# Kernel optimization log

Measured on AMD Instinct MI355X. Metric: run time of the kernel, lower is better.

## Reference

```python
import jax, jax.numpy as jnp
import numpy as np

B, T, D, H = 64, 196, 768, 3072
WBIT_MAX = 127.0          # int8 symmetric weight range
BIAS_MAX = 2.0 ** 31 - 1  # bias_bit = 32


def round_ste(v):
    # straight-through rounding (QAT semantics)
    return v + jax.lax.stop_gradient(jnp.round(v) - v)


def quant_linear(x, w, b, a_s, relu_clip):
    # symmetric per-tensor int8 weight quantization
    w_s = jnp.max(jnp.abs(w)) / WBIT_MAX
    w_int = jnp.clip(round_ste(w / w_s), -WBIT_MAX, WBIT_MAX)
    # bias quantized at the accumulator scale a_s * w_s (int32 range)
    b_int = jnp.clip(round_ste(b / (w_s * a_s)), -BIAS_MAX, BIAS_MAX)
    out = jnp.einsum('btd,hd->bth', x, w_int) + b_int  # integer-domain accumulation
    if relu_clip:
        out = jax.nn.relu(out)
    return out, w_s, a_s * w_s


def setup_inputs() -> dict:
    key = jax.random.key(0)
    ks = jax.random.split(key, 6)
    x = jnp.round(jax.random.normal(ks[0], (B, T, D), dtype=jnp.float32) * 20.0)  # int8-like activations
    w1 = jax.random.normal(ks[1], (H, D), dtype=jnp.float32) * 0.02
    b1 = jax.random.normal(ks[2], (H,), dtype=jnp.float32) * 0.02
    w2 = jax.random.normal(ks[3], (D, H), dtype=jnp.float32) * 0.02
    b2 = jax.random.normal(ks[4], (D,), dtype=jnp.float32) * 0.02
    a_s = jax.random.uniform(ks[5], (1,), dtype=jnp.float32, minval=0.01, maxval=0.05)
    return {"x": x, "w1": w1, "b1": b1, "w2": w2, "b2": b2, "a_s": a_s}


def reference(x, w1, b1, w2, b2, a_s):
    s = a_s[0]
    # fc1: quantized linear, no activation clip
    h, w_s1, s = quant_linear(x, w1, b1, s, relu_clip=False)
    # fc2: quantized linear with ReLU clip
    out, w_s2, s = quant_linear(h, w2, b2, s, relu_clip=True)
    return (out, s)
```

## Files before the change

### kernel.cpp

```cpp
#include <hip/hip_runtime.h>
#include <hip/hip_bf16.h>
#include <type_traits>

typedef __attribute__((ext_vector_type(4))) float f32x4;
typedef __attribute__((ext_vector_type(4))) int   i32x4;

static __device__ __forceinline__ void stage16(const void* g, void* l) {
  __builtin_amdgcn_global_load_lds((const __attribute__((address_space(1))) void*)g,
                                   (__attribute__((address_space(3))) void*)l,
                                   16, 0, 0);
}

__global__ void prep_kernel(const float4* __restrict__ x, uchar4* __restrict__ xq, int n4x,
                            const float4* __restrict__ w1, const float4* __restrict__ w2,
                            int n4w, unsigned* __restrict__ mx) {
  if (blockIdx.y == 0) {
    const int stride = gridDim.x * blockDim.x;
    for (int i = blockIdx.x * blockDim.x + threadIdx.x; i < n4x; i += stride) {
      float4 v = x[i];
      uchar4 o;
      o.x = (unsigned char)(char)fminf(fmaxf(v.x, -127.f), 127.f);
      o.y = (unsigned char)(char)fminf(fmaxf(v.y, -127.f), 127.f);
      o.z = (unsigned char)(char)fminf(fmaxf(v.z, -127.f), 127.f);
      o.w = (unsigned char)(char)fminf(fmaxf(v.w, -127.f), 127.f);
      xq[i] = o;
    }
  } else {
    if (blockIdx.x >= 96) return;
    __shared__ unsigned red[4];
    const float4* w = (blockIdx.y == 1) ? w1 : w2;
    unsigned m = 0;
    const int stride = 96 * 256;
    for (int i = blockIdx.x * blockDim.x + threadIdx.x; i < n4w; i += stride) {
      float4 v = w[i];
      unsigned a;
      a = __float_as_uint(fabsf(v.x)); m = m > a ? m : a;
      a = __float_as_uint(fabsf(v.y)); m = m > a ? m : a;
      a = __float_as_uint(fabsf(v.z)); m = m > a ? m : a;
      a = __float_as_uint(fabsf(v.w)); m = m > a ? m : a;
    }
#pragma unroll
    for (int off = 32; off > 0; off >>= 1) {
      unsigned t = (unsigned)__shfl_down((int)m, off, 64);
      m = m > t ? m : t;
    }
    if ((threadIdx.x & 63) == 0) red[threadIdx.x >> 6] = m;
    __syncthreads();
    if (threadIdx.x == 0) {
      unsigned t0 = red[0] > red[1] ? red[0] : red[1];
      unsigned t1 = red[2] > red[3] ? red[2] : red[3];
      atomicMax(mx + blockIdx.y - 1, t0 > t1 ? t0 : t1);
    }
  }
}

__global__ void quantwb_kernel(const float* __restrict__ w1, const float* __restrict__ w2,
                               unsigned char* __restrict__ w1q, unsigned* __restrict__ w2qw,
                               const float* __restrict__ b1, const float* __restrict__ b2,
                               float* __restrict__ b1i, float* __restrict__ b2i,
                               const unsigned* __restrict__ mx, const float* __restrict__ a_s,
                               float* __restrict__ s_out, int n4, int H, int D) {
  const float ws1 = __uint_as_float(mx[0]) / 127.0f;
  const float ws2 = __uint_as_float(mx[1]) / 127.0f;
  const int stride = gridDim.x * blockDim.x;
  if (blockIdx.y == 0) {
    const float4* w = (const float4*)w1;
    uchar4* wq = (uchar4*)w1q;
    for (int i = blockIdx.x * blockDim.x + threadIdx.x; i < n4; i += stride) {
      float4 v = w[i];
      uchar4 o;
      o.x = (unsigned char)(char)fminf(fmaxf(rintf(v.x / ws1), -127.f), 127.f);
      o.y = (unsigned char)(char)fminf(fmaxf(rintf(v.y / ws1), -127.f), 127.f);
      o.z = (unsigned char)(char)fminf(fmaxf(rintf(v.z / ws1), -127.f), 127.f);
      o.w = (unsigned char)(char)fminf(fmaxf(rintf(v.w / ws1), -127.f), 127.f);
      wq[i] = o;
    }
  } else if (blockIdx.y == 1) {
    const int ndw = n4;
    const int dpr = H >> 2;
    for (int g = blockIdx.x * blockDim.x + threadIdx.x; g < ndw; g += stride) {
      const int n = g / dpr;
      const int d = g - n * dpr;
      const int grp = d >> 4, dl = d & 15;
      const float* src = w2 + (size_t)n * H + grp * 64 + dl;
      unsigned r = 0;
#pragma unroll
      for (int i = 0; i < 4; ++i) {
        float v = src[i * 16];
        int q = (int)fminf(fmaxf(rintf(v / ws2), -127.f), 127.f);
        r |= ((unsigned)q & 0xFFu) << (i * 8);
      }
      w2qw[g] = r;
    }
  } else {
    if (blockIdx.x != 0) return;
    const float s0 = a_s[0];
    const float s1 = s0 * ws1;
    const float d1 = ws1 * s0;
    const float d2 = ws2 * s1;
    if (threadIdx.x == 0) s_out[0] = s1 * ws2;
    for (int i = threadIdx.x; i < H; i += blockDim.x) {
      float q = rintf(b1[i] / d1);
      b1i[i] = fminf(fmaxf(q, -2147483647.f), 2147483647.f);
    }
    for (int i = threadIdx.x; i < D; i += blockDim.x) {
      float q = rintf(b2[i] / d2);
      b2i[i] = fminf(fmaxf(q, -2147483647.f), 2147483647.f);
    }
  }
}


__global__ __launch_bounds__(256) void gemm_fc1(
    const char* __restrict__ A, const char* __restrict__ Bt,
    const float* __restrict__ b1f, unsigned char* __restrict__ hq,
    float* __restrict__ stab, int M, int N, int Kb)
{
  __shared__ char lds[2 * 32768];
  const int tid = threadIdx.x;
  const int lane = tid & 63;
  const int wave = tid >> 6;
  const int wr = wave >> 1;
  const int wc = wave & 1;

  const int nbx = M / 128;
  const int nby = N / 128;
  const int bandSize = 16 * nby;
  const int b = blockIdx.x / bandSize;
  const int local = blockIdx.x - b * bandSize;
  const int r0 = b * 16;
  const int rn = min(16, nbx - r0);
  const int c = local / rn;
  const int r = r0 + (local - c * rn);
  const int row0 = r * 128;
  const int col0 = c * 128;

  const int srw = tid >> 3;
  const int chunk = (tid & 7) ^ (srw & 7);
  const char* Ag = A + (size_t)(row0 + srw) * Kb + chunk * 16;
  const char* Bg = Bt + (size_t)(col0 + srw) * Kb + chunk * 16;
  const int stA = wave * 1024;
  const int stB = 16384 + wave * 1024;

  auto stage = [&](int slot, int h) {
    const int hb = h << 7;
    char* da = lds + slot * 32768 + stA;
    char* db = lds + slot * 32768 + stB;
#pragma unroll
    for (int i = 0; i < 4; ++i)
      stage16(Ag + hb + (size_t)(i * 32) * Kb, da + i * 4096);
#pragma unroll
    for (int i = 0; i < 4; ++i)
      stage16(Bg + hb + (size_t)(i * 32) * Kb, db + i * 4096);
  };

  i32x4 acc[4][4];
#pragma unroll
  for (int i = 0; i < 4; ++i)
#pragma unroll
    for (int j = 0; j < 4; ++j) acc[i][j] = (i32x4)(0);

  const int nS = Kb >> 7;
  stage(0, 0);
  stage(1, 1);
  asm volatile("s_waitcnt vmcnt(8)" ::: "memory");
  __builtin_amdgcn_s_barrier();

  const int fr = lane & 15;
  const int fg = lane >> 4;
  const int xw = (fg ^ (fr & 7)) << 4;
  const int aoff = (wr * 64 + fr) * 128 + xw;
  const int boff = 16384 + (wc * 64 + fr) * 128 + xw;

  for (int t = 0; t < nS; ++t) {
    const int so = (t & 1) * 32768;
    i32x4 af[2][4], bf[2][4];
#pragma unroll
    for (int h = 0; h < 2; ++h) {
      const int hx = h << 6;
#pragma unroll
      for (int mi = 0; mi < 4; ++mi)
        af[h][mi] = *(const i32x4*)(lds + so + ((aoff ^ hx) + mi * 2048));
#pragma unroll
      for (int ni = 0; ni < 4; ++ni)
        bf[h][ni] = *(const i32x4*)(lds + so + ((boff ^ hx) + ni * 2048));
    }
    asm volatile("s_waitcnt lgkmcnt(0)" ::: "memory");
    __builtin_amdgcn_sched_barrier(0);
    __builtin_amdgcn_s_barrier();
    if (t + 2 < nS) stage(t & 1, t + 2);
    __builtin_amdgcn_s_setprio(1);
#pragma unroll
    for (int h = 0; h < 2; ++h)
#pragma unroll
      for (int mi = 0; mi < 4; ++mi)
#pragma unroll
        for (int ni = 0; ni < 4; ++ni)
          acc[mi][ni] = __builtin_amdgcn_mfma_i32_16x16x64_i8(
              af[h][mi], bf[h][ni], acc[mi][ni], 0, 0, 0);
    __builtin_amdgcn_s_setprio(0);
    if (t + 2 < nS) asm volatile("s_waitcnt vmcnt(8)" ::: "memory");
    else            asm volatile("s_waitcnt vmcnt(0)" ::: "memory");
    __builtin_amdgcn_s_barrier();
  }

  __syncthreads();
  float* rowtab = (float*)lds;
  const int orow_l = wr * 64 + fg * 4;
  const int ocol_l = wc * 64 + fr;
  float bv[4];
#pragma unroll
  for (int nf = 0; nf < 4; ++nf) bv[nf] = b1f[col0 + ocol_l + nf * 16];

#pragma unroll
  for (int mf = 0; mf < 4; ++mf) {
    float rmax[4] = {0.f, 0.f, 0.f, 0.f};
#pragma unroll
    for (int nf = 0; nf < 4; ++nf)
#pragma unroll
      for (int rg = 0; rg < 4; ++rg) {
        float v = (float)acc[mf][nf][rg] + bv[nf];
        rmax[rg] = fmaxf(rmax[rg], fabsf(v));
      }
#pragma unroll
    for (int rg = 0; rg < 4; ++rg) {
#pragma unroll
      for (int m = 1; m <= 8; m <<= 1)
        rmax[rg] = fmaxf(rmax[rg], __shfl_xor(rmax[rg], m, 64));
      if (fr == 0) rowtab[(orow_l + mf * 16 + rg) * 2 + wc] = rmax[rg];
    }
  }
  __syncthreads();
#pragma unroll
  for (int mf = 0; mf < 4; ++mf) {
#pragma unroll
    for (int rg = 0; rg < 4; ++rg) {
      const int lr = orow_l + mf * 16 + rg;
      float rm = fmaxf(rowtab[lr * 2], rowtab[lr * 2 + 1]);
      float inv = rm > 0.f ? 127.f / rm : 0.f;
      if (wc == 0 && fr == 0) stab[(size_t)(row0 + lr) * 24 + c] = rm * (1.f / 127.f);
      unsigned pk = 0;
#pragma unroll
      for (int nf = 0; nf < 4; ++nf) {
        float v = (float)acc[mf][nf][rg] + bv[nf];
        int q = (int)rintf(v * inv);
        pk |= ((unsigned)q & 0xFFu) << (nf * 8);
      }
      *(unsigned*)(hq + (size_t)(row0 + lr) * N + col0 + wc * 64 + fr * 4) = pk;
    }
  }
}

__global__ void requant_kernel(const uint4* __restrict__ hq, uint4* __restrict__ hq2,
                               const float* __restrict__ stab, float* __restrict__ srow,
                               int Mrows) {
  const int row = blockIdx.x * 4 + (threadIdx.x >> 6);
  if (row >= Mrows) return;
  const int lane = threadIdx.x & 63;
  const float* st = stab + (size_t)row * 24;
  float sr = 0.f;
#pragma unroll
  for (int i = 0; i < 24; ++i) sr = fmaxf(sr, st[i]);
  if (lane == 0) srow[row] = sr;
  const float rinv = sr > 0.f ? 1.f / sr : 0.f;
  const uint4* in = hq + (size_t)row * 192;
  uint4* outp = hq2 + (size_t)row * 192;
#pragma unroll
  for (int it = 0; it < 3; ++it) {
    const int j = lane + it * 64;
    const float ratio = st[j >> 3] * rinv;
    uint4 iv = in[j], ov;
    unsigned* ip = (unsigned*)&iv;
    unsigned* op = (unsigned*)&ov;
#pragma unroll
    for (int w = 0; w < 4; ++w) {
      unsigned rr = 0;
#pragma unroll
      for (int k = 0; k < 4; ++k) {
        int q = (int)(signed char)((ip[w] >> (k * 8)) & 0xFF);
        int nq = (int)rintf((float)q * ratio);
        rr |= ((unsigned)nq & 0xFF) << (k * 8);
      }
      op[w] = rr;
    }
    outp[j] = ov;
  }
}

__global__ __launch_bounds__(256) void gemm_fc2(
    const char* __restrict__ A, const char* __restrict__ Bt,
    const float* __restrict__ bias, const float* __restrict__ srow,
    float* __restrict__ Cout, int M, int N, int Kb)
{
  __shared__ char lds[2 * 32768];
  const int tid = threadIdx.x;
  const int lane = tid & 63;
  const int wave = tid >> 6;
  const int wr = wave >> 1;
  const int wc = wave & 1;

  const int nbx = M / 128;
  const int nby = N / 128;
  const int nwg = nbx * nby;
  const int q8 = nwg >> 3, r8 = nwg & 7;
  const int xcd = blockIdx.x & 7, bidx = blockIdx.x >> 3;
  const int wg = (xcd < r8 ? xcd * (q8 + 1) : r8 * (q8 + 1) + (xcd - r8) * q8) + bidx;
  const int r = wg / nby;
  const int c = wg % nby;
  const int row0 = r * 128;
  const int col0 = c * 128;

  const int srw = tid >> 3;
  const int chunk = (tid & 7) ^ (srw & 7);
  const char* Ag = A + (size_t)(row0 + srw) * Kb + chunk * 16;
  const char* Bg = Bt + (size_t)(col0 + srw) * Kb + chunk * 16;
  const int stA = wave * 1024;
  const int stB = 16384 + wave * 1024;

  auto stage = [&](int slot, int h) {
    const int hb = h << 7;
    char* da = lds + slot * 32768 + stA;
    char* db = lds + slot * 32768 + stB;
#pragma unroll
    for (int i = 0; i < 4; ++i)
      stage16(Ag + hb + (size_t)(i * 32) * Kb, da + i * 4096);
#pragma unroll
    for (int i = 0; i < 4; ++i)
      stage16(Bg + hb + (size_t)(i * 32) * Kb, db + i * 4096);
  };

  i32x4 acc[4][4];
#pragma unroll
  for (int i = 0; i < 4; ++i)
#pragma unroll
    for (int j = 0; j < 4; ++j) acc[i][j] = (i32x4)(0);

  const int nS = Kb >> 7;
  stage(0, 0);
  stage(1, 1);
  asm volatile("s_waitcnt vmcnt(8)" ::: "memory");
  __builtin_amdgcn_s_barrier();

  const int fr = lane & 15;
  const int fg = lane >> 4;
  const int xw = (fg ^ (fr & 7)) << 4;
  const int aoff = (wr * 64 + fr) * 128 + xw;
  const int boff = 16384 + (wc * 64 + fr) * 128 + xw;

  for (int t = 0; t < nS; ++t) {
    const int so = (t & 1) * 32768;
    i32x4 af[2][4], bf[2][4];
#pragma unroll
    for (int h = 0; h < 2; ++h) {
      const int hx = h << 6;
#pragma unroll
      for (int mi = 0; mi < 4; ++mi)
        af[h][mi] = *(const i32x4*)(lds + so + ((aoff ^ hx) + mi * 2048));
#pragma unroll
      for (int ni = 0; ni < 4; ++ni)
        bf[h][ni] = *(const i32x4*)(lds + so + ((boff ^ hx) + ni * 2048));
    }
    asm volatile("s_waitcnt lgkmcnt(0)" ::: "memory");
    __builtin_amdgcn_sched_barrier(0);
    __builtin_amdgcn_s_barrier();
    if (t + 2 < nS) stage(t & 1, t + 2);
    __builtin_amdgcn_s_setprio(1);
#pragma unroll
    for (int h = 0; h < 2; ++h)
#pragma unroll
      for (int mi = 0; mi < 4; ++mi)
#pragma unroll
        for (int ni = 0; ni < 4; ++ni)
          acc[mi][ni] = __builtin_amdgcn_mfma_i32_16x16x64_i8(
              af[h][mi], bf[h][ni], acc[mi][ni], 0, 0, 0);
    __builtin_amdgcn_s_setprio(0);
    if (t + 2 < nS) asm volatile("s_waitcnt vmcnt(8)" ::: "memory");
    else            asm volatile("s_waitcnt vmcnt(0)" ::: "memory");
    __builtin_amdgcn_s_barrier();
  }

  const int orow = row0 + wr * 64 + fg * 4;
  const int ocol = col0 + wc * 64 + fr;
#pragma unroll
  for (int mi = 0; mi < 4; ++mi) {
    float sr[4];
#pragma unroll
    for (int rg = 0; rg < 4; ++rg) sr[rg] = srow[orow + mi * 16 + rg];
#pragma unroll
    for (int ni = 0; ni < 4; ++ni) {
      const int col = ocol + ni * 16;
      const float bv = bias[col];
#pragma unroll
      for (int rg = 0; rg < 4; ++rg) {
        float v = sr[rg] * (float)acc[mi][ni][rg] + bv;
        Cout[(size_t)(orow + mi * 16 + rg) * N + col] = fmaxf(v, 0.f);
      }
    }
  }
}


extern "C" void kernel_launch(void* const* d_in, const int* in_sizes, int n_in,
                              void* d_out, int out_size, void* d_ws, size_t ws_size,
                              hipStream_t stream) {
  const float* x  = (const float*)d_in[0];
  const float* w1 = (const float*)d_in[1];
  const float* b1 = (const float*)d_in[2];
  const float* w2 = (const float*)d_in[3];
  const float* b2 = (const float*)d_in[4];
  const float* as = (const float*)d_in[5];

  const int Mrows = 64 * 196;
  const int D = 768, H = 3072;

  char* ws = (char*)d_ws;
  size_t off = 0;
  auto align256 = [](size_t v) { return (v + 255) & ~(size_t)255; };
  unsigned* mx = (unsigned*)(ws + off); off += 256;
  char* xq8    = (char*)(ws + off);     off += align256((size_t)Mrows * D);
  char* w1q8   = (char*)(ws + off);     off += align256((size_t)H * D);
  char* w2q8   = (char*)(ws + off);     off += align256((size_t)D * H);
  float* b1i = (float*)(ws + off); off += align256((size_t)H * 4);
  float* b2i = (float*)(ws + off); off += align256((size_t)D * 4);
  float* stab = (float*)(ws + off); off += align256((size_t)Mrows * 24 * 4);
  float* srow = (float*)(ws + off); off += align256((size_t)Mrows * 4);
  unsigned char* hq  = (unsigned char*)(ws + off); off += align256((size_t)Mrows * H);
  unsigned char* hq2 = (unsigned char*)(ws + off); off += align256((size_t)Mrows * H);
  if (off > ws_size) return;

  float* out = (float*)d_out;
  float* s_out = out + (out_size - 1);

  hipMemsetAsync(mx, 0, 8, stream);

  const int nw4 = H * D / 4;
  prep_kernel<<<dim3(1024, 3), dim3(256), 0, stream>>>(
      (const float4*)x, (uchar4*)xq8, Mrows * D / 4,
      (const float4*)w1, (const float4*)w2, nw4, mx);
  quantwb_kernel<<<dim3(1024, 3), dim3(256), 0, stream>>>(
      w1, w2, (unsigned char*)w1q8, (unsigned*)w2q8,
      b1, b2, b1i, b2i, mx, as, s_out, nw4, H, D);

  gemm_fc1<<<dim3((Mrows / 128) * (H / 128)), dim3(256), 0, stream>>>(
      xq8, w1q8, b1i, hq, stab, Mrows, H, D);
  requant_kernel<<<dim3(Mrows / 4), dim3(256), 0, stream>>>(
      (const uint4*)hq, (uint4*)hq2, stab, srow, Mrows);
  gemm_fc2<<<dim3((Mrows / 128) * (D / 128)), dim3(256), 0, stream>>>(
      (const char*)hq2, w2q8, b2i, srow, out, Mrows, D, H);
}
```

Before: 147.2 us.

## Single-buffer fc1 GEMM and move activation quantization into quantwb kernel

The fc1 GEMM drops its double-buffered LDS pipeline, where the next tile was prefetched while the current one was computed. It now loads one 32KB K-tile per iteration, synchronizes, runs the MFMAs, then synchronizes again, and keeps a separate 1KB region for the row-max table. The smaller LDS footprint could allow more blocks per CU, but global loads no longer overlap with compute, and there are two full barriers per K step. Separately, the x-to-int8 conversion moves from the max-reduction kernel into the quantwb kernel as a new grid row, so the reduction kernel launches only 96x2 blocks.

```diff
diff --git a/kernel.cpp b/kernel.cpp
--- a/kernel.cpp
+++ b/kernel.cpp
@@ -11,51 +11,37 @@
                                    16, 0, 0);
 }
 
-__global__ void prep_kernel(const float4* __restrict__ x, uchar4* __restrict__ xq, int n4x,
-                            const float4* __restrict__ w1, const float4* __restrict__ w2,
+__global__ void prep_kernel(const float4* __restrict__ w1, const float4* __restrict__ w2,
                             int n4w, unsigned* __restrict__ mx) {
-  if (blockIdx.y == 0) {
-    const int stride = gridDim.x * blockDim.x;
-    for (int i = blockIdx.x * blockDim.x + threadIdx.x; i < n4x; i += stride) {
-      float4 v = x[i];
-      uchar4 o;
-      o.x = (unsigned char)(char)fminf(fmaxf(v.x, -127.f), 127.f);
-      o.y = (unsigned char)(char)fminf(fmaxf(v.y, -127.f), 127.f);
-      o.z = (unsigned char)(char)fminf(fmaxf(v.z, -127.f), 127.f);
-      o.w = (unsigned char)(char)fminf(fmaxf(v.w, -127.f), 127.f);
-      xq[i] = o;
-    }
-  } else {
-    if (blockIdx.x >= 96) return;
-    __shared__ unsigned red[4];
-    const float4* w = (blockIdx.y == 1) ? w1 : w2;
-    unsigned m = 0;
-    const int stride = 96 * 256;
-    for (int i = blockIdx.x * blockDim.x + threadIdx.x; i < n4w; i += stride) {
-      float4 v = w[i];
-      unsigned a;
-      a = __float_as_uint(fabsf(v.x)); m = m > a ? m : a;
-      a = __float_as_uint(fabsf(v.y)); m = m > a ? m : a;
-      a = __float_as_uint(fabsf(v.z)); m = m > a ? m : a;
-      a = __float_as_uint(fabsf(v.w)); m = m > a ? m : a;
-    }
-#pragma unroll
-    for (int off = 32; off > 0; off >>= 1) {
-      unsigned t = (unsigned)__shfl_down((int)m, off, 64);
-      m = m > t ? m : t;
-    }
-    if ((threadIdx.x & 63) == 0) red[threadIdx.x >> 6] = m;
-    __syncthreads();
-    if (threadIdx.x == 0) {
-      unsigned t0 = red[0] > red[1] ? red[0] : red[1];
-      unsigned t1 = red[2] > red[3] ? red[2] : red[3];
-      atomicMax(mx + blockIdx.y - 1, t0 > t1 ? t0 : t1);
-    }
+  __shared__ unsigned red[4];
+  const float4* w = blockIdx.y ? w2 : w1;
+  unsigned m = 0;
+  const int stride = gridDim.x * blockDim.x;
+  for (int i = blockIdx.x * blockDim.x + threadIdx.x; i < n4w; i += stride) {
+    float4 v = w[i];
+    unsigned a;
+    a = __float_as_uint(fabsf(v.x)); m = m > a ? m : a;
+    a = __float_as_uint(fabsf(v.y)); m = m > a ? m : a;
+    a = __float_as_uint(fabsf(v.z)); m = m > a ? m : a;
+    a = __float_as_uint(fabsf(v.w)); m = m > a ? m : a;
+  }
+#pragma unroll
+  for (int off = 32; off > 0; off >>= 1) {
+    unsigned t = (unsigned)__shfl_down((int)m, off, 64);
+    m = m > t ? m : t;
+  }
+  if ((threadIdx.x & 63) == 0) red[threadIdx.x >> 6] = m;
+  __syncthreads();
+  if (threadIdx.x == 0) {
+    unsigned t0 = red[0] > red[1] ? red[0] : red[1];
+    unsigned t1 = red[2] > red[3] ? red[2] : red[3];
+    atomicMax(mx + blockIdx.y, t0 > t1 ? t0 : t1);
   }
 }
 
 __global__ void quantwb_kernel(const float* __restrict__ w1, const float* __restrict__ w2,
                                unsigned char* __restrict__ w1q, unsigned* __restrict__ w2qw,
+                               const float4* __restrict__ x, uchar4* __restrict__ xq, int n4x,
                                const float* __restrict__ b1, const float* __restrict__ b2,
                                float* __restrict__ b1i, float* __restrict__ b2i,
                                const unsigned* __restrict__ mx, const float* __restrict__ a_s,
@@ -92,6 +78,16 @@
       }
       w2qw[g] = r;
     }
+  } else if (blockIdx.y == 2) {
+    for (int i = blockIdx.x * blockDim.x + threadIdx.x; i < n4x; i += stride) {
+      float4 v = x[i];
+      uchar4 o;
+      o.x = (unsigned char)(char)fminf(fmaxf(v.x, -127.f), 127.f);
+      o.y = (unsigned char)(char)fminf(fmaxf(v.y, -127.f), 127.f);
+      o.z = (unsigned char)(char)fminf(fmaxf(v.z, -127.f), 127.f);
+      o.w = (unsigned char)(char)fminf(fmaxf(v.w, -127.f), 127.f);
+      xq[i] = o;
+    }
   } else {
     if (blockIdx.x != 0) return;
     const float s0 = a_s[0];
@@ -116,7 +112,7 @@
     const float* __restrict__ b1f, unsigned char* __restrict__ hq,
     float* __restrict__ stab, int M, int N, int Kb)
 {
-  __shared__ char lds[2 * 32768];
+  __shared__ char lds[32768 + 1024];
   const int tid = threadIdx.x;
   const int lane = tid & 63;
   const int wave = tid >> 6;
@@ -139,56 +135,47 @@
   const int chunk = (tid & 7) ^ (srw & 7);
   const char* Ag = A + (size_t)(row0 + srw) * Kb + chunk * 16;
   const char* Bg = Bt + (size_t)(col0 + srw) * Kb + chunk * 16;
-  const int stA = wave * 1024;
-  const int stB = 16384 + wave * 1024;
-
-  auto stage = [&](int slot, int h) {
-    const int hb = h << 7;
-    char* da = lds + slot * 32768 + stA;
-    char* db = lds + slot * 32768 + stB;
-#pragma unroll
-    for (int i = 0; i < 4; ++i)
-      stage16(Ag + hb + (size_t)(i * 32) * Kb, da + i * 4096);
-#pragma unroll
-    for (int i = 0; i < 4; ++i)
-      stage16(Bg + hb + (size_t)(i * 32) * Kb, db + i * 4096);
-  };
+  char* const stAp = lds + wave * 1024;
+  char* const stBp = lds + 16384 + wave * 1024;
 
   i32x4 acc[4][4];
 #pragma unroll
   for (int i = 0; i < 4; ++i)
 #pragma unroll
     for (int j = 0; j < 4; ++j) acc[i][j] = (i32x4)(0);
-
-  const int nS = Kb >> 7;
-  stage(0, 0);
-  stage(1, 1);
-  asm volatile("s_waitcnt vmcnt(8)" ::: "memory");
-  __builtin_amdgcn_s_barrier();
 
   const int fr = lane & 15;
   const int fg = lane >> 4;
+  const int ocol_l = wc * 64 + fr;
+  float bv[4];
+#pragma unroll
+  for (int nf = 0; nf < 4; ++nf) bv[nf] = b1f[col0 + ocol_l + nf * 16];
+
   const int xw = (fg ^ (fr & 7)) << 4;
   const int aoff = (wr * 64 + fr) * 128 + xw;
   const int boff = 16384 + (wc * 64 + fr) * 128 + xw;
 
+  const int nS = Kb >> 7;
   for (int t = 0; t < nS; ++t) {
-    const int so = (t & 1) * 32768;
+    const int hb = t << 7;
+#pragma unroll
+    for (int i = 0; i < 4; ++i)
+      stage16(Ag + hb + (size_t)(i * 32) * Kb, stAp + i * 4096);
+#pragma unroll
+    for (int i = 0; i < 4; ++i)
+      stage16(Bg + hb + (size_t)(i * 32) * Kb, stBp + i * 4096);
+    __syncthreads();
     i32x4 af[2][4], bf[2][4];
 #pragma unroll
     for (int h = 0; h < 2; ++h) {
       const int hx = h << 6;
 #pragma unroll
       for (int mi = 0; mi < 4; ++mi)
-        af[h][mi] = *(const i32x4*)(lds + so + ((aoff ^ hx) + mi * 2048));
+        af[h][mi] = *(const i32x4*)(lds + ((aoff ^ hx) + mi * 2048));
 #pragma unroll
       for (int ni = 0; ni < 4; ++ni)
-        bf[h][ni] = *(const i32x4*)(lds + so + ((boff ^ hx) + ni * 2048));
-    }
-    asm volatile("s_waitcnt lgkmcnt(0)" ::: "memory");
-    __builtin_amdgcn_sched_barrier(0);
-    __builtin_amdgcn_s_barrier();
-    if (t + 2 < nS) stage(t & 1, t + 2);
+        bf[h][ni] = *(const i32x4*)(lds + ((boff ^ hx) + ni * 2048));
+    }
     __builtin_amdgcn_s_setprio(1);
 #pragma unroll
     for (int h = 0; h < 2; ++h)
@@ -199,18 +186,11 @@
           acc[mi][ni] = __builtin_amdgcn_mfma_i32_16x16x64_i8(
               af[h][mi], bf[h][ni], acc[mi][ni], 0, 0, 0);
     __builtin_amdgcn_s_setprio(0);
-    if (t + 2 < nS) asm volatile("s_waitcnt vmcnt(8)" ::: "memory");
-    else            asm volatile("s_waitcnt vmcnt(0)" ::: "memory");
-    __builtin_amdgcn_s_barrier();
-  }
-
-  __syncthreads();
-  float* rowtab = (float*)lds;
+    __syncthreads();
+  }
+
+  float* rowtab = (float*)(lds + 32768);
   const int orow_l = wr * 64 + fg * 4;
-  const int ocol_l = wc * 64 + fr;
-  float bv[4];
-#pragma unroll
-  for (int nf = 0; nf < 4; ++nf) bv[nf] = b1f[col0 + ocol_l + nf * 16];
 
 #pragma unroll
   for (int mf = 0; mf < 4; ++mf) {
@@ -434,11 +414,11 @@
   hipMemsetAsync(mx, 0, 8, stream);
 
   const int nw4 = H * D / 4;
-  prep_kernel<<<dim3(1024, 3), dim3(256), 0, stream>>>(
+  prep_kernel<<<dim3(96, 2), dim3(256), 0, stream>>>(
+      (const float4*)w1, (const float4*)w2, nw4, mx);
+  quantwb_kernel<<<dim3(1024, 4), dim3(256), 0, stream>>>(
+      w1, w2, (unsigned char*)w1q8, (unsigned*)w2q8,
       (const float4*)x, (uchar4*)xq8, Mrows * D / 4,
-      (const float4*)w1, (const float4*)w2, nw4, mx);
-  quantwb_kernel<<<dim3(1024, 3), dim3(256), 0, stream>>>(
-      w1, w2, (unsigned char*)w1q8, (unsigned*)w2q8,
       b1, b2, b1i, b2i, mx, as, s_out, nw4, H, D);
 
   gemm_fc1<<<dim3((Mrows / 128) * (H / 128)), dim3(256), 0, stream>>>(
```

Result: faster. 143.9 us (-2.2%).
